# Kernel optimization log

Hardware: AMD Instinct MI355X
Metric: run time of the kernel (lower is better)

The kernel has to match this reference:

```python
import jax, jax.numpy as jnp
import numpy as np

B, C, H, W = 4, 128, 96, 96
OC = 128          # out_channels
K = 3             # kernel_size
OFF = 2 * K * K   # offset channels = 18
PAD = 1
EPS = 1e-6


def conv2d(x, w, b, pad=1, groups=1):
    out = jax.lax.conv_general_dilated(
        x, w, window_strides=(1, 1), padding=[(pad, pad), (pad, pad)],
        dimension_numbers=('NCHW', 'OIHW', 'NCHW'), feature_group_count=groups)
    return out + b[None, :, None, None]


def bilinear_gather(x, ys, xs):
    # x: [B,C,H,W]; ys, xs: [B,H,W] float sample coords. Zero outside bounds.
    Bn, Cn, Hn, Wn = x.shape
    xflat = x.reshape(Bn, Cn, Hn * Wn)
    y0 = jnp.floor(ys)
    x0 = jnp.floor(xs)
    out = jnp.zeros((Bn, Cn, Hn, Wn), dtype=x.dtype)
    for dy, dx in ((0, 0), (0, 1), (1, 0), (1, 1)):
        yy = y0 + dy
        xx = x0 + dx
        w = (1.0 - jnp.abs(ys - yy)) * (1.0 - jnp.abs(xs - xx))
        valid = (yy >= 0) & (yy < Hn) & (xx >= 0) & (xx < Wn)
        yi = jnp.clip(yy, 0, Hn - 1).astype(jnp.int32)
        xi = jnp.clip(xx, 0, Wn - 1).astype(jnp.int32)
        idx = (yi * Wn + xi).reshape(Bn, 1, Hn * Wn)
        g = jnp.take_along_axis(xflat, idx, axis=2).reshape(Bn, Cn, Hn, Wn)
        out = out + (w * valid)[:, None] * g
    return out


def deform_conv(x, offsets, w, b):
    # torchvision DeformConv2d v1: offsets [B, 2*K*K, H, W], pairs (dy, dx) per tap
    Bn, Cn, Hn, Wn = x.shape
    off = offsets.reshape(Bn, K * K, 2, Hn, Wn)
    gy, gx = jnp.meshgrid(jnp.arange(Hn, dtype=x.dtype),
                          jnp.arange(Wn, dtype=x.dtype), indexing='ij')
    acc = jnp.zeros((Bn, w.shape[0], Hn, Wn), dtype=x.dtype)
    for k in range(K * K):
        ky, kx = k // K, k % K
        ys = gy[None] - PAD + ky + off[:, k, 0]
        xs = gx[None] - PAD + kx + off[:, k, 1]
        samp = bilinear_gather(x, ys, xs)                 # [B,C,H,W]
        acc = acc + jnp.einsum('bchw,oc->bohw', samp, w[:, :, ky, kx])
    return acc + b[None, :, None, None]


def setup_inputs() -> dict:
    key = jax.random.key(0)
    ks = jax.random.split(key, 8)
    s = 0.05
    return {
        'x': jax.random.normal(ks[0], (B, C, H, W), jnp.float32),
        'w_off': jax.random.normal(ks[1], (OFF, C, K, K), jnp.float32) * s,
        'b_off': jnp.zeros((OFF,), jnp.float32),
        'w_def': jax.random.normal(ks[2], (OC, C, K, K), jnp.float32) * s,
        'b_def': jnp.zeros((OC,), jnp.float32),
        'ln_w': jnp.ones((OC,), jnp.float32),
        'ln_b': jnp.zeros((OC,), jnp.float32),
        'w_dw': jax.random.normal(ks[3], (C, 1, 3, 3), jnp.float32) * s,
        'b_dw': jnp.zeros((C,), jnp.float32),
        'w_pw': jax.random.normal(ks[4], (OC, C, 1, 1), jnp.float32) * s,
        'b_pw': jnp.zeros((OC,), jnp.float32),
    }


def reference(x, w_off, b_off, w_def, b_def, ln_w, ln_b, w_dw, b_dw, w_pw, b_pw):
    offsets = conv2d(x, w_off, b_off, pad=PAD)            # [B,18,H,W]
    x1 = deform_conv(x, offsets, w_def, b_def)            # [B,OC,H,W]
    # channels-first LayerNorm
    u = x1.mean(1, keepdims=True)
    s = ((x1 - u) ** 2).mean(1, keepdims=True)
    x1 = ln_w[None, :, None, None] * ((x1 - u) / jnp.sqrt(s + EPS)) \
         + ln_b[None, :, None, None]
    x2 = conv2d(x, w_dw, b_dw, pad=1, groups=C)           # depthwise 3x3
    x4 = conv2d(x2 + x, w_pw, b_pw, pad=0)                # pointwise 1x1
    x4 = jax.nn.silu(x4)
    return x1 + x4
```

## Files before the change

### kernel.cpp

```cpp
#include <hip/hip_runtime.h>
#include <hip/hip_bf16.h>
#include <stdint.h>

#define BN 4
#define CN 128
#define HN 96
#define WN 96
#define HW (HN*WN)
#define OCN 128
#define OFFC 18
#define EPSV 1e-6f
#define HP 98
#define WP 98

typedef __attribute__((ext_vector_type(8))) short bf16x8;
typedef __attribute__((ext_vector_type(4))) float f32x4;

__device__ __forceinline__ float lo16(uint32_t u) {
  union { uint32_t i; float f; } v; v.i = u << 16; return v.f;
}
__device__ __forceinline__ float hi16(uint32_t u) {
  union { uint32_t i; float f; } v; v.i = u & 0xffff0000u; return v.f;
}
__device__ __forceinline__ uint16_t f2b(float f) {
  union { float f; uint32_t i; } u; u.f = f;
  uint32_t r = u.i + 0x7fffu + ((u.i >> 16) & 1u);
  return (uint16_t)(r >> 16);
}
__device__ __forceinline__ uint32_t pk2(float a, float b) {
  return (uint32_t)f2b(a) | ((uint32_t)f2b(b) << 16);
}
__device__ __forceinline__ int swz(int row, int c) { return c ^ ((row & 7) << 3); }

__device__ __align__(16) uint16_t g_def[9 * 128 * 128];
__device__ __align__(16) uint16_t g_pw[128 * 128];
__device__ __align__(16) uint16_t g_off[32 * 1152];
__device__ __align__(16) uint16_t g_xp[(size_t)BN * HP * WP * CN];

__global__ __launch_bounds__(256)
void k_prep_w(const float* __restrict__ w_def, const float* __restrict__ w_pw,
              const float* __restrict__ w_off) {
  int i = blockIdx.x * 256 + threadIdx.x;
  if (i < 147456) {
    int k = i >> 14, rem = i & 16383, oc = rem >> 7, c = rem & 127;
    g_def[i] = f2b(w_def[((oc << 7) + c) * 9 + k]);
  } else if (i < 147456 + 16384) {
    int j = i - 147456;
    g_pw[j] = f2b(w_pw[j]);
  } else if (i < 147456 + 16384 + 36864) {
    int j = i - 163840;
    int row = j / 1152, col = j - row * 1152;
    int kk = col >> 7, c = col & 127;
    g_off[j] = (row < OFFC) ? f2b(w_off[((row << 7) + c) * 9 + kk]) : (uint16_t)0;
  }
}

__global__ __launch_bounds__(256)
void k_prep_x(const float* __restrict__ x) {
  __shared__ uint16_t trans[96][136];
  int blk = blockIdx.x;
  int y1 = blk % HP;
  int b  = blk / HP;
  int t = (int)threadIdx.x;
  uint16_t* dst = g_xp + ((size_t)(b * HP + y1) * WP) * CN;
  if (y1 == 0 || y1 == HP - 1) {
    for (int i = t; i < WP * CN / 8; i += 256)
      ((uint4*)dst)[i] = make_uint4(0, 0, 0, 0);
    return;
  }
  int y = y1 - 1;
  for (int i = t; i < CN * WN / 4; i += 256) {
    int c = i / 24, xq = i - c * 24;
    float4 f = *(const float4*)&x[((size_t)(b * CN + c) * HN + y) * WN + xq * 4];
    trans[xq * 4 + 0][c] = f2b(f.x);
    trans[xq * 4 + 1][c] = f2b(f.y);
    trans[xq * 4 + 2][c] = f2b(f.z);
    trans[xq * 4 + 3][c] = f2b(f.w);
  }
  __syncthreads();
  for (int i = t; i < 2 * CN / 8; i += 256) {
    int side = i >> 4, j = i & 15;
    ((uint4*)(dst + (size_t)side * (WP - 1) * CN))[j] = make_uint4(0, 0, 0, 0);
  }
  for (int i = t; i < WN * CN / 8; i += 256) {
    int xw = i >> 4, cq = (i & 15) * 8;
    ((uint4*)(dst + CN))[i] = *(const uint4*)&trans[xw][cq];
  }
}

__global__ __launch_bounds__(256, 3)
void k_fused(const float* __restrict__ b_off, const float* __restrict__ b_def,
             const float* __restrict__ ln_w, const float* __restrict__ ln_b,
             const float* __restrict__ w_dw, const float* __restrict__ b_dw,
             const float* __restrict__ b_pw, float* __restrict__ out) {
  __shared__ __align__(16) uint16_t patch[3 * 34 * 128];
  __shared__ float offarena[576];
  float (*offl)[32] = (float (*)[32])offarena;
  float (*red1)[32] = (float (*)[32])offarena;
  float (*red2)[32] = (float (*)[32])(offarena + 128);
  float* muv = offarena + 256;
  float* rsv = offarena + 288;
  uint16_t* samp0 = patch;
  uint16_t* samp1 = patch + 4096;
  uint16_t* dwT   = patch + 8192;

  int bid = blockIdx.x;
  int wid = (bid & 7) * 144 + (bid >> 3);
  int wt = wid % 3;
  int h  = (wid / 3) % HN;
  int b  = wid / (3 * HN);
  int w0 = wt * 32;

  int t = (int)threadIdx.x;
  int l = t & 63, w = t >> 6;
  int g = l >> 4, fr = l & 15;
  int p = t & 31, cg = t >> 5;
  const uint16_t* xb = g_xp + (size_t)b * HP * WP * CN;
  int cbase = w * 32 + (l & 3) * 8;
  const uint16_t* bp = xb + cbase;

  #pragma unroll
  for (int rep = 0; rep < 7; ++rep) {
    int e = t + 256 * rep;
    if (e < 1632) {
      int rec = e >> 4, chunk = e & 15;
      int ky = rec / 34, i = rec - 34 * ky;
      const uint16_t* src = xb + ((size_t)(h + ky) * WP + (w0 + i)) * CN + chunk * 8;
      *(uint4*)&patch[((ky * 34 + i) << 7) + swz(i, chunk * 8)] = *(const uint4*)src;
    }
  }
  __syncthreads();

  {
    int toc = w >> 1, tp = w & 1;
    f32x4 aco = {0.f, 0.f, 0.f, 0.f};
    #pragma unroll
    for (int ks = 0; ks < 36; ++ks) {
      int kk = ks >> 2;
      int ky = kk / 3, kx = kk - 3 * ky;
      int cb = ((ks & 3) << 5) + (g << 3);
      int i = fr + (tp << 4) + kx;
      bf16x8 a = *(const bf16x8*)&g_off[(toc * 16 + fr) * 1152 + (ks << 5) + (g << 3)];
      bf16x8 bb = *(const bf16x8*)&patch[((ky * 34 + i) << 7) + swz(i, cb)];
      aco = __builtin_amdgcn_mfma_f32_16x16x32_bf16(a, bb, aco, 0, 0, 0);
    }
    #pragma unroll
    for (int reg = 0; reg < 4; ++reg) {
      int j = toc * 16 + g * 4 + reg;
      if (j < OFFC) offl[j][(tp << 4) + fr] = aco[reg] + b_off[j];
    }
  }

  float adw[16];
  {
    #pragma unroll
    for (int cl = 0; cl < 16; ++cl) adw[cl] = b_dw[cg * 16 + cl];
    #pragma unroll
    for (int ky = 0; ky < 3; ++ky) {
      #pragma unroll
      for (int kx = 0; kx < 3; ++kx) {
        int i = p + kx;
        uint32_t r[8];
        *(uint4*)&r[0] = *(const uint4*)&patch[((ky * 34 + i) << 7) + swz(i, cg * 16)];
        *(uint4*)&r[4] = *(const uint4*)&patch[((ky * 34 + i) << 7) + swz(i, cg * 16 + 8)];
        #pragma unroll
        for (int c2 = 0; c2 < 8; ++c2) {
          adw[2 * c2]     += lo16(r[c2]) * w_dw[(cg * 16 + 2 * c2) * 9 + ky * 3 + kx];
          adw[2 * c2 + 1] += hi16(r[c2]) * w_dw[(cg * 16 + 2 * c2 + 1) * 9 + ky * 3 + kx];
        }
      }
    }
    int i = p + 1;
    uint32_t r[8];
    *(uint4*)&r[0] = *(const uint4*)&patch[((34 + i) << 7) + swz(i, cg * 16)];
    *(uint4*)&r[4] = *(const uint4*)&patch[((34 + i) << 7) + swz(i, cg * 16 + 8)];
    #pragma unroll
    for (int c2 = 0; c2 < 8; ++c2) {
      adw[2 * c2]     += lo16(r[c2]);
      adw[2 * c2 + 1] += hi16(r[c2]);
    }
  }
  __syncthreads();

  auto GATHER = [&](int kk, uint16_t* wb) {
    int ky = kk / 3, kx = kk - 3 * ky;
    #pragma unroll
    for (int half = 0; half < 2; ++half) {
      int px = half * 16 + (l >> 2);
      float dy = offl[2 * kk][px], dx = offl[2 * kk + 1][px];
      float ys = (float)(h - 1 + ky) + dy;
      float xs = (float)(w0 + px - 1 + kx) + dx;
      float y0f = floorf(ys), x0f = floorf(xs);
      float fy = ys - y0f, fx = xs - x0f;
      int y0 = (int)y0f, x0 = (int)x0f;
      float w00 = (1.f - fy) * (1.f - fx), w01 = (1.f - fy) * fx;
      float w10 = fy * (1.f - fx),         w11 = fy * fx;
      bool yok0 = (y0 >= 0) & (y0 < HN), yok1 = (y0 + 1 >= 0) & (y0 + 1 < HN);
      bool xok0 = (x0 >= 0) & (x0 < WN), xok1 = (x0 + 1 >= 0) & (x0 + 1 < WN);
      if (!(yok0 & xok0)) w00 = 0.f;
      if (!(yok0 & xok1)) w01 = 0.f;
      if (!(yok1 & xok0)) w10 = 0.f;
      if (!(yok1 & xok1)) w11 = 0.f;
      int ya  = min(max(y0, -1), HN) + 1;
      int yb2 = min(max(y0 + 1, -1), HN) + 1;
      int xa  = min(max(x0, -1), WN) + 1;
      int xc2 = min(max(x0 + 1, -1), WN) + 1;
      uint32_t A[4], B[4], C[4], D[4];
      *(uint4*)A = *(const uint4*)(bp + ((size_t)ya * WP + xa) * CN);
      *(uint4*)B = *(const uint4*)(bp + ((size_t)ya * WP + xc2) * CN);
      *(uint4*)C = *(const uint4*)(bp + ((size_t)yb2 * WP + xa) * CN);
      *(uint4*)D = *(const uint4*)(bp + ((size_t)yb2 * WP + xc2) * CN);
      uint32_t pk4[4];
      #pragma unroll
      for (int q2 = 0; q2 < 4; ++q2) {
        float s0 = w00 * lo16(A[q2]) + w01 * lo16(B[q2]) + w10 * lo16(C[q2]) + w11 * lo16(D[q2]);
        float s1 = w00 * hi16(A[q2]) + w01 * hi16(B[q2]) + w10 * hi16(C[q2]) + w11 * hi16(D[q2]);
        pk4[q2] = pk2(s0, s1);
      }
      *(uint4*)&wb[(px << 7) + swz(px, cbase)] = *(uint4*)pk4;
    }
  };

  {
    #pragma unroll
    for (int m = 0; m < 2; ++m) {
      uint4 u = { pk2(adw[8*m+0], adw[8*m+1]), pk2(adw[8*m+2], adw[8*m+3]),
                  pk2(adw[8*m+4], adw[8*m+5]), pk2(adw[8*m+6], adw[8*m+7]) };
      *(uint4*)&dwT[(p << 7) + swz(p, cg * 16 + 8 * m)] = u;
    }
    GATHER(0, samp0);
  }
  __syncthreads();

  f32x4 a4[2][2];
  #pragma unroll
  for (int q1 = 0; q1 < 2; ++q1)
    #pragma unroll
    for (int q2 = 0; q2 < 2; ++q2) a4[q1][q2] = (f32x4){0.f, 0.f, 0.f, 0.f};
  {
    #pragma unroll
    for (int ks = 0; ks < 4; ++ks) {
      int kb = (ks << 5) + (g << 3);
      bf16x8 a0 = *(const bf16x8*)&g_pw[(32 * w + fr) * 128 + kb];
      bf16x8 a1 = *(const bf16x8*)&g_pw[(32 * w + 16 + fr) * 128 + kb];
      #pragma unroll
      for (int tp2 = 0; tp2 < 2; ++tp2) {
        int pp = (tp2 << 4) + fr;
        bf16x8 bb = *(const bf16x8*)&dwT[(pp << 7) + swz(pp, kb)];
        a4[0][tp2] = __builtin_amdgcn_mfma_f32_16x16x32_bf16(a0, bb, a4[0][tp2], 0, 0, 0);
        a4[1][tp2] = __builtin_amdgcn_mfma_f32_16x16x32_bf16(a1, bb, a4[1][tp2], 0, 0, 0);
      }
    }
    #pragma unroll
    for (int toc2 = 0; toc2 < 2; ++toc2)
      #pragma unroll
      for (int tp2 = 0; tp2 < 2; ++tp2)
        #pragma unroll
        for (int reg = 0; reg < 4; ++reg) {
          int oc = 32 * w + 16 * toc2 + 4 * g + reg;
          float v = a4[toc2][tp2][reg] + b_pw[oc];
          a4[toc2][tp2][reg] = v / (1.f + __expf(-v));
        }
  }
  __syncthreads();

  f32x4 ac1[2][2];
  #pragma unroll
  for (int q1 = 0; q1 < 2; ++q1)
    #pragma unroll
    for (int q2 = 0; q2 < 2; ++q2) ac1[q1][q2] = (f32x4){0.f, 0.f, 0.f, 0.f};

  #pragma unroll 1
  for (int k = 0; k < 9; ++k) {
    uint16_t* rb = (k & 1) ? samp1 : samp0;
    uint16_t* wb = (k & 1) ? samp0 : samp1;
    if (k < 8) GATHER(k + 1, wb);
    {
      const uint16_t* gdk = g_def + (k << 14);
      #pragma unroll
      for (int ks = 0; ks < 4; ++ks) {
        int kb = (ks << 5) + (g << 3);
        bf16x8 a0 = *(const bf16x8*)&gdk[(32 * w + fr) * 128 + kb];
        bf16x8 a1 = *(const bf16x8*)&gdk[(32 * w + 16 + fr) * 128 + kb];
        #pragma unroll
        for (int tp2 = 0; tp2 < 2; ++tp2) {
          int pp = (tp2 << 4) + fr;
          bf16x8 bb = *(const bf16x8*)&rb[(pp << 7) + swz(pp, kb)];
          ac1[0][tp2] = __builtin_amdgcn_mfma_f32_16x16x32_bf16(a0, bb, ac1[0][tp2], 0, 0, 0);
          ac1[1][tp2] = __builtin_amdgcn_mfma_f32_16x16x32_bf16(a1, bb, ac1[1][tp2], 0, 0, 0);
        }
      }
    }
    __syncthreads();
  }

  #pragma unroll
  for (int toc2 = 0; toc2 < 2; ++toc2)
    #pragma unroll
    for (int tp2 = 0; tp2 < 2; ++tp2)
      #pragma unroll
      for (int reg = 0; reg < 4; ++reg) {
        int oc = 32 * w + 16 * toc2 + 4 * g + reg;
        ac1[toc2][tp2][reg] += b_def[oc];
      }
  {
    float s1[2], s2[2];
    #pragma unroll
    for (int tp2 = 0; tp2 < 2; ++tp2) {
      float a = 0.f, q = 0.f;
      #pragma unroll
      for (int toc2 = 0; toc2 < 2; ++toc2)
        #pragma unroll
        for (int reg = 0; reg < 4; ++reg) {
          float v = ac1[toc2][tp2][reg];
          a += v; q += v * v;
        }
      a += __shfl_xor(a, 16); a += __shfl_xor(a, 32);
      q += __shfl_xor(q, 16); q += __shfl_xor(q, 32);
      s1[tp2] = a; s2[tp2] = q;
    }
    if (l < 16) {
      red1[w][l] = s1[0]; red1[w][l + 16] = s1[1];
      red2[w][l] = s2[0]; red2[w][l + 16] = s2[1];
    }
  }
  __syncthreads();
  if (t < 32) {
    float m = (red1[0][t] + red1[1][t] + red1[2][t] + red1[3][t]) * (1.f / 128.f);
    float q = (red2[0][t] + red2[1][t] + red2[2][t] + red2[3][t]) * (1.f / 128.f) - m * m;
    muv[t] = m;
    rsv[t] = rsqrtf(q + EPSV);
  }
  __syncthreads();
  {
    #pragma unroll
    for (int toc2 = 0; toc2 < 2; ++toc2)
      #pragma unroll
      for (int tp2 = 0; tp2 < 2; ++tp2) {
        int pp = (tp2 << 4) + fr;
        float mm = muv[pp], rr = rsv[pp];
        #pragma unroll
        for (int reg = 0; reg < 4; ++reg) {
          int oc = 32 * w + 16 * toc2 + 4 * g + reg;
          float v = (ac1[toc2][tp2][reg] - mm) * rr * ln_w[oc] + ln_b[oc]
                    + a4[toc2][tp2][reg];
          out[((size_t)(b * OCN + oc) * HN + h) * WN + w0 + pp] = v;
        }
      }
  }
}

extern "C" void kernel_launch(void* const* d_in, const int* in_sizes, int n_in,
                              void* d_out, int out_size, void* d_ws, size_t ws_size,
                              hipStream_t stream) {
  const float* x     = (const float*)d_in[0];
  const float* w_off = (const float*)d_in[1];
  const float* b_off = (const float*)d_in[2];
  const float* w_def = (const float*)d_in[3];
  const float* b_def = (const float*)d_in[4];
  const float* ln_w  = (const float*)d_in[5];
  const float* ln_b  = (const float*)d_in[6];
  const float* w_dw  = (const float*)d_in[7];
  const float* b_dw  = (const float*)d_in[8];
  const float* w_pw  = (const float*)d_in[9];
  const float* b_pw  = (const float*)d_in[10];
  float* out = (float*)d_out;

  hipLaunchKernelGGL(k_prep_w, dim3(784), dim3(256), 0, stream, w_def, w_pw, w_off);
  hipLaunchKernelGGL(k_prep_x, dim3(BN * HP), dim3(256), 0, stream, x);
  hipLaunchKernelGGL(k_fused, dim3(BN * HN * 3), dim3(256), 0, stream,
                     b_off, b_def, ln_w, ln_b, w_dw, b_dw, b_pw, out);
}
```

Measured before the change: 116.7 us.

## Split deform conv reduction over channels per wave with private LDS buffers

Each wave now gathers and multiplies only its own 32-channel slice across all 128 output channels, using per-wave sample buffers. This removes the block-wide barrier after every tap. Partial sums are then reduced across the four waves through LDS in four serialized phases. In exchange each wave holds 64 accumulator floats, which raises register pressure, and the launch-bounds occupancy hint is dropped. The reduction also adds LDS traffic and extra barriers.

```diff
diff --git a/kernel.cpp b/kernel.cpp
--- a/kernel.cpp
+++ b/kernel.cpp
@@ -12,6 +12,7 @@
 #define EPSV 1e-6f
 #define HP 98
 #define WP 98
+#define NWG (BN*HN*3)
 
 typedef __attribute__((ext_vector_type(8))) short bf16x8;
 typedef __attribute__((ext_vector_type(4))) float f32x4;
@@ -88,21 +89,20 @@
   }
 }
 
-__global__ __launch_bounds__(256, 3)
+__global__ __launch_bounds__(256)
 void k_fused(const float* __restrict__ b_off, const float* __restrict__ b_def,
              const float* __restrict__ ln_w, const float* __restrict__ ln_b,
              const float* __restrict__ w_dw, const float* __restrict__ b_dw,
              const float* __restrict__ b_pw, float* __restrict__ out) {
-  __shared__ __align__(16) uint16_t patch[3 * 34 * 128];
+  __shared__ __align__(16) uint16_t patch[13056];
+  __shared__ __align__(16) uint16_t dwT[4096];
   __shared__ float offarena[576];
   float (*offl)[32] = (float (*)[32])offarena;
   float (*red1)[32] = (float (*)[32])offarena;
   float (*red2)[32] = (float (*)[32])(offarena + 128);
   float* muv = offarena + 256;
   float* rsv = offarena + 288;
-  uint16_t* samp0 = patch;
-  uint16_t* samp1 = patch + 4096;
-  uint16_t* dwT   = patch + 8192;
+  float* redbuf = (float*)patch;
 
   int bid = blockIdx.x;
   int wid = (bid & 7) * 144 + (bid >> 3);
@@ -118,6 +118,8 @@
   const uint16_t* xb = g_xp + (size_t)b * HP * WP * CN;
   int cbase = w * 32 + (l & 3) * 8;
   const uint16_t* bp = xb + cbase;
+  uint16_t* sbuf0 = patch + w * 1280;
+  uint16_t* sbuf1 = patch + 5120 + w * 1280;
 
   #pragma unroll
   for (int rep = 0; rep < 7; ++rep) {
@@ -184,6 +186,7 @@
 
   auto GATHER = [&](int kk, uint16_t* wb) {
     int ky = kk / 3, kx = kk - 3 * ky;
+    int chunk = l & 3;
     #pragma unroll
     for (int half = 0; half < 2; ++half) {
       int px = half * 16 + (l >> 2);
@@ -217,7 +220,24 @@
         float s1 = w00 * hi16(A[q2]) + w01 * hi16(B[q2]) + w10 * hi16(C[q2]) + w11 * hi16(D[q2]);
         pk4[q2] = pk2(s0, s1);
       }
-      *(uint4*)&wb[(px << 7) + swz(px, cbase)] = *(uint4*)pk4;
+      *(uint4*)&wb[px * 40 + chunk * 8] = *(uint4*)pk4;
+    }
+  };
+
+  f32x4 acc[8][2];
+  #pragma unroll
+  for (int r = 0; r < 8; ++r)
+    #pragma unroll
+    for (int q2 = 0; q2 < 2; ++q2) acc[r][q2] = (f32x4){0.f, 0.f, 0.f, 0.f};
+  auto TAPMM = [&](int k, const uint16_t* rb) {
+    const uint16_t* gdk = g_def + (k << 14) + w * 32 + g * 8;
+    bf16x8 b0 = *(const bf16x8*)&rb[fr * 40 + g * 8];
+    bf16x8 b1 = *(const bf16x8*)&rb[(16 + fr) * 40 + g * 8];
+    #pragma unroll
+    for (int r = 0; r < 8; ++r) {
+      bf16x8 a = *(const bf16x8*)&gdk[(16 * r + fr) * 128];
+      acc[r][0] = __builtin_amdgcn_mfma_f32_16x16x32_bf16(a, b0, acc[r][0], 0, 0, 0);
+      acc[r][1] = __builtin_amdgcn_mfma_f32_16x16x32_bf16(a, b1, acc[r][1], 0, 0, 0);
     }
   };
 
@@ -228,7 +248,7 @@
                   pk2(adw[8*m+4], adw[8*m+5]), pk2(adw[8*m+6], adw[8*m+7]) };
       *(uint4*)&dwT[(p << 7) + swz(p, cg * 16 + 8 * m)] = u;
     }
-    GATHER(0, samp0);
+    GATHER(0, sbuf0);
   }
   __syncthreads();
 
@@ -262,47 +282,47 @@
           a4[toc2][tp2][reg] = v / (1.f + __expf(-v));
         }
   }
-  __syncthreads();
+
+  #pragma unroll 1
+  for (int k = 0; k < 9; ++k) {
+    uint16_t* rb = (k & 1) ? sbuf1 : sbuf0;
+    uint16_t* wb = (k & 1) ? sbuf0 : sbuf1;
+    if (k < 8) GATHER(k + 1, wb);
+    TAPMM(k, rb);
+  }
+  __syncthreads();
+
+  #pragma unroll 1
+  for (int ph = 0; ph < 4; ++ph) {
+    if (w == ph) {
+      #pragma unroll
+      for (int r = 0; r < 8; ++r)
+        #pragma unroll
+        for (int tp2 = 0; tp2 < 2; ++tp2)
+          #pragma unroll
+          for (int reg = 0; reg < 4; ++reg) {
+            int oc = 16 * r + g * 4 + reg;
+            int px = 16 * tp2 + fr;
+            int idx = oc * 33 + px;
+            if (ph == 0) redbuf[idx] = acc[r][tp2][reg];
+            else         redbuf[idx] += acc[r][tp2][reg];
+          }
+    }
+    __syncthreads();
+  }
 
   f32x4 ac1[2][2];
   #pragma unroll
-  for (int q1 = 0; q1 < 2; ++q1)
-    #pragma unroll
-    for (int q2 = 0; q2 < 2; ++q2) ac1[q1][q2] = (f32x4){0.f, 0.f, 0.f, 0.f};
-
-  #pragma unroll 1
-  for (int k = 0; k < 9; ++k) {
-    uint16_t* rb = (k & 1) ? samp1 : samp0;
-    uint16_t* wb = (k & 1) ? samp0 : samp1;
-    if (k < 8) GATHER(k + 1, wb);
-    {
-      const uint16_t* gdk = g_def + (k << 14);
-      #pragma unroll
-      for (int ks = 0; ks < 4; ++ks) {
-        int kb = (ks << 5) + (g << 3);
-        bf16x8 a0 = *(const bf16x8*)&gdk[(32 * w + fr) * 128 + kb];
-        bf16x8 a1 = *(const bf16x8*)&gdk[(32 * w + 16 + fr) * 128 + kb];
-        #pragma unroll
-        for (int tp2 = 0; tp2 < 2; ++tp2) {
-          int pp = (tp2 << 4) + fr;
-          bf16x8 bb = *(const bf16x8*)&rb[(pp << 7) + swz(pp, kb)];
-          ac1[0][tp2] = __builtin_amdgcn_mfma_f32_16x16x32_bf16(a0, bb, ac1[0][tp2], 0, 0, 0);
-          ac1[1][tp2] = __builtin_amdgcn_mfma_f32_16x16x32_bf16(a1, bb, ac1[1][tp2], 0, 0, 0);
-        }
-      }
-    }
-    __syncthreads();
-  }
-
-  #pragma unroll
   for (int toc2 = 0; toc2 < 2; ++toc2)
     #pragma unroll
     for (int tp2 = 0; tp2 < 2; ++tp2)
       #pragma unroll
       for (int reg = 0; reg < 4; ++reg) {
         int oc = 32 * w + 16 * toc2 + 4 * g + reg;
-        ac1[toc2][tp2][reg] += b_def[oc];
-      }
+        int px = 16 * tp2 + fr;
+        ac1[toc2][tp2][reg] = redbuf[oc * 33 + px] + b_def[oc];
+      }
+
   {
     float s1[2], s2[2];
     #pragma unroll
@@ -319,6 +339,7 @@
       q += __shfl_xor(q, 16); q += __shfl_xor(q, 32);
       s1[tp2] = a; s2[tp2] = q;
     }
+    __syncthreads();
     if (l < 16) {
       red1[w][l] = s1[0]; red1[w][l + 16] = s1[1];
       red2[w][l] = s2[0]; red2[w][l + 16] = s2[1];
@@ -368,6 +389,6 @@
 
   hipLaunchKernelGGL(k_prep_w, dim3(784), dim3(256), 0, stream, w_def, w_pw, w_off);
   hipLaunchKernelGGL(k_prep_x, dim3(BN * HP), dim3(256), 0, stream, x);
-  hipLaunchKernelGGL(k_fused, dim3(BN * HN * 3), dim3(256), 0, stream,
+  hipLaunchKernelGGL(k_fused, dim3(NWG), dim3(256), 0, stream,
                      b_off, b_def, ln_w, ln_b, w_dw, b_dw, b_pw, out);
 }
```

Measured after the change: 216.5 us. 85.5% more time.

## Process two output rows per workgroup to reuse patch rows and weight fragments

Applied to the files above, without the earlier changes.

Each workgroup now computes two adjacent output rows instead of one. It loads a 4-row input patch shared by both rows and reuses the deform-conv weight fragments across the two rows inside an 18-step gather/MFMA pipeline. The aim is to cut redundant patch loads and weight reads from global memory and to halve the number of workgroups. In exchange it uses more registers and LDS, and the occupancy hint drops from 3 to 2 blocks per CU, with only 576 workgroups left to fill the GPU.

```diff
diff --git a/kernel.cpp b/kernel.cpp
--- a/kernel.cpp
+++ b/kernel.cpp
@@ -12,6 +12,7 @@
 #define EPSV 1e-6f
 #define HP 98
 #define WP 98
+#define NWG2 (BN*(HN/2)*3)
 
 typedef __attribute__((ext_vector_type(8))) short bf16x8;
 typedef __attribute__((ext_vector_type(4))) float f32x4;
@@ -88,27 +89,24 @@
   }
 }
 
-__global__ __launch_bounds__(256, 3)
+__global__ __launch_bounds__(256, 2)
 void k_fused(const float* __restrict__ b_off, const float* __restrict__ b_def,
              const float* __restrict__ ln_w, const float* __restrict__ ln_b,
              const float* __restrict__ w_dw, const float* __restrict__ b_dw,
              const float* __restrict__ b_pw, float* __restrict__ out) {
-  __shared__ __align__(16) uint16_t patch[3 * 34 * 128];
-  __shared__ float offarena[576];
-  float (*offl)[32] = (float (*)[32])offarena;
-  float (*red1)[32] = (float (*)[32])offarena;
-  float (*red2)[32] = (float (*)[32])(offarena + 128);
-  float* muv = offarena + 256;
-  float* rsv = offarena + 288;
-  uint16_t* samp0 = patch;
-  uint16_t* samp1 = patch + 4096;
-  uint16_t* dwT   = patch + 8192;
+  __shared__ __align__(16) uint16_t patch[4 * 34 * 128];
+  __shared__ float offarena[1152];
+
+  uint16_t* dwT   = patch;
+  uint16_t* samp0 = patch + 8192;
+  uint16_t* samp1 = patch + 12288;
 
   int bid = blockIdx.x;
-  int wid = (bid & 7) * 144 + (bid >> 3);
+  int wid = (bid & 7) * (NWG2 / 8) + (bid >> 3);
   int wt = wid % 3;
-  int h  = (wid / 3) % HN;
-  int b  = wid / (3 * HN);
+  int h2 = (wid / 3) % (HN / 2);
+  int b  = wid / (3 * (HN / 2));
+  int h  = 2 * h2;
   int w0 = wt * 32;
 
   int t = (int)threadIdx.x;
@@ -120,9 +118,9 @@
   const uint16_t* bp = xb + cbase;
 
   #pragma unroll
-  for (int rep = 0; rep < 7; ++rep) {
+  for (int rep = 0; rep < 9; ++rep) {
     int e = t + 256 * rep;
-    if (e < 1632) {
+    if (e < 2176) {
       int rec = e >> 4, chunk = e & 15;
       int ky = rec / 34, i = rec - 34 * ky;
       const uint16_t* src = xb + ((size_t)(h + ky) * WP + (w0 + i)) * CN + chunk * 8;
@@ -132,63 +130,71 @@
   __syncthreads();
 
   {
-    int toc = w >> 1, tp = w & 1;
-    f32x4 aco = {0.f, 0.f, 0.f, 0.f};
+    int t1 = w >> 1, toc = w & 1;
+    f32x4 aco0 = {0.f,0.f,0.f,0.f}, aco1 = {0.f,0.f,0.f,0.f};
     #pragma unroll
     for (int ks = 0; ks < 36; ++ks) {
       int kk = ks >> 2;
       int ky = kk / 3, kx = kk - 3 * ky;
       int cb = ((ks & 3) << 5) + (g << 3);
-      int i = fr + (tp << 4) + kx;
       bf16x8 a = *(const bf16x8*)&g_off[(toc * 16 + fr) * 1152 + (ks << 5) + (g << 3)];
-      bf16x8 bb = *(const bf16x8*)&patch[((ky * 34 + i) << 7) + swz(i, cb)];
-      aco = __builtin_amdgcn_mfma_f32_16x16x32_bf16(a, bb, aco, 0, 0, 0);
+      int i0 = fr + kx, i1 = fr + 16 + kx;
+      bf16x8 bb0 = *(const bf16x8*)&patch[(((t1 + ky) * 34 + i0) << 7) + swz(i0, cb)];
+      bf16x8 bb1 = *(const bf16x8*)&patch[(((t1 + ky) * 34 + i1) << 7) + swz(i1, cb)];
+      aco0 = __builtin_amdgcn_mfma_f32_16x16x32_bf16(a, bb0, aco0, 0, 0, 0);
+      aco1 = __builtin_amdgcn_mfma_f32_16x16x32_bf16(a, bb1, aco1, 0, 0, 0);
     }
     #pragma unroll
     for (int reg = 0; reg < 4; ++reg) {
       int j = toc * 16 + g * 4 + reg;
-      if (j < OFFC) offl[j][(tp << 4) + fr] = aco[reg] + b_off[j];
-    }
-  }
-
-  float adw[16];
-  {
-    #pragma unroll
-    for (int cl = 0; cl < 16; ++cl) adw[cl] = b_dw[cg * 16 + cl];
+      if (j < OFFC) {
+        offarena[t1 * 576 + j * 32 + fr]      = aco0[reg] + b_off[j];
+        offarena[t1 * 576 + j * 32 + 16 + fr] = aco1[reg] + b_off[j];
+      }
+    }
+  }
+
+  float adw0[16], adw1[16];
+  auto DW = [&](float (&A)[16], int t2) {
+    #pragma unroll
+    for (int cl = 0; cl < 16; ++cl) A[cl] = b_dw[cg * 16 + cl];
     #pragma unroll
     for (int ky = 0; ky < 3; ++ky) {
       #pragma unroll
       for (int kx = 0; kx < 3; ++kx) {
-        int i = p + kx;
+        int i = p + kx, row = t2 + ky;
         uint32_t r[8];
-        *(uint4*)&r[0] = *(const uint4*)&patch[((ky * 34 + i) << 7) + swz(i, cg * 16)];
-        *(uint4*)&r[4] = *(const uint4*)&patch[((ky * 34 + i) << 7) + swz(i, cg * 16 + 8)];
+        *(uint4*)&r[0] = *(const uint4*)&patch[((row * 34 + i) << 7) + swz(i, cg * 16)];
+        *(uint4*)&r[4] = *(const uint4*)&patch[((row * 34 + i) << 7) + swz(i, cg * 16 + 8)];
         #pragma unroll
         for (int c2 = 0; c2 < 8; ++c2) {
-          adw[2 * c2]     += lo16(r[c2]) * w_dw[(cg * 16 + 2 * c2) * 9 + ky * 3 + kx];
-          adw[2 * c2 + 1] += hi16(r[c2]) * w_dw[(cg * 16 + 2 * c2 + 1) * 9 + ky * 3 + kx];
+          A[2 * c2]     += lo16(r[c2]) * w_dw[(cg * 16 + 2 * c2) * 9 + ky * 3 + kx];
+          A[2 * c2 + 1] += hi16(r[c2]) * w_dw[(cg * 16 + 2 * c2 + 1) * 9 + ky * 3 + kx];
         }
       }
     }
-    int i = p + 1;
+    int i = p + 1, row = t2 + 1;
     uint32_t r[8];
-    *(uint4*)&r[0] = *(const uint4*)&patch[((34 + i) << 7) + swz(i, cg * 16)];
-    *(uint4*)&r[4] = *(const uint4*)&patch[((34 + i) << 7) + swz(i, cg * 16 + 8)];
+    *(uint4*)&r[0] = *(const uint4*)&patch[((row * 34 + i) << 7) + swz(i, cg * 16)];
+    *(uint4*)&r[4] = *(const uint4*)&patch[((row * 34 + i) << 7) + swz(i, cg * 16 + 8)];
     #pragma unroll
     for (int c2 = 0; c2 < 8; ++c2) {
-      adw[2 * c2]     += lo16(r[c2]);
-      adw[2 * c2 + 1] += hi16(r[c2]);
-    }
-  }
-  __syncthreads();
-
-  auto GATHER = [&](int kk, uint16_t* wb) {
+      A[2 * c2]     += lo16(r[c2]);
+      A[2 * c2 + 1] += hi16(r[c2]);
+    }
+  };
+  DW(adw0, 0);
+  DW(adw1, 1);
+  __syncthreads();
+
+  auto GATHER = [&](int kk, int t2, uint16_t* wb) {
     int ky = kk / 3, kx = kk - 3 * ky;
     #pragma unroll
     for (int half = 0; half < 2; ++half) {
       int px = half * 16 + (l >> 2);
-      float dy = offl[2 * kk][px], dx = offl[2 * kk + 1][px];
-      float ys = (float)(h - 1 + ky) + dy;
+      float dy = offarena[t2 * 576 + (2 * kk) * 32 + px];
+      float dx = offarena[t2 * 576 + (2 * kk + 1) * 32 + px];
+      float ys = (float)(h + t2 - 1 + ky) + dy;
       float xs = (float)(w0 + px - 1 + kx) + dx;
       float y0f = floorf(ys), x0f = floorf(xs);
       float fy = ys - y0f, fx = xs - x0f;
@@ -224,87 +230,117 @@
   {
     #pragma unroll
     for (int m = 0; m < 2; ++m) {
-      uint4 u = { pk2(adw[8*m+0], adw[8*m+1]), pk2(adw[8*m+2], adw[8*m+3]),
-                  pk2(adw[8*m+4], adw[8*m+5]), pk2(adw[8*m+6], adw[8*m+7]) };
-      *(uint4*)&dwT[(p << 7) + swz(p, cg * 16 + 8 * m)] = u;
-    }
-    GATHER(0, samp0);
-  }
-  __syncthreads();
-
-  f32x4 a4[2][2];
+      uint4 u0 = { pk2(adw0[8*m+0], adw0[8*m+1]), pk2(adw0[8*m+2], adw0[8*m+3]),
+                   pk2(adw0[8*m+4], adw0[8*m+5]), pk2(adw0[8*m+6], adw0[8*m+7]) };
+      *(uint4*)&dwT[(p << 7) + swz(p, cg * 16 + 8 * m)] = u0;
+      uint4 u1 = { pk2(adw1[8*m+0], adw1[8*m+1]), pk2(adw1[8*m+2], adw1[8*m+3]),
+                   pk2(adw1[8*m+4], adw1[8*m+5]), pk2(adw1[8*m+6], adw1[8*m+7]) };
+      *(uint4*)&dwT[4096 + (p << 7) + swz(p, cg * 16 + 8 * m)] = u1;
+    }
+    GATHER(0, 0, samp0);
+  }
+  __syncthreads();
+
+  f32x4 a4T0[2][2], a4T1[2][2];
   #pragma unroll
   for (int q1 = 0; q1 < 2; ++q1)
     #pragma unroll
-    for (int q2 = 0; q2 < 2; ++q2) a4[q1][q2] = (f32x4){0.f, 0.f, 0.f, 0.f};
+    for (int q2 = 0; q2 < 2; ++q2) {
+      a4T0[q1][q2] = (f32x4){0.f,0.f,0.f,0.f};
+      a4T1[q1][q2] = (f32x4){0.f,0.f,0.f,0.f};
+    }
   {
     #pragma unroll
     for (int ks = 0; ks < 4; ++ks) {
       int kb = (ks << 5) + (g << 3);
-      bf16x8 a0 = *(const bf16x8*)&g_pw[(32 * w + fr) * 128 + kb];
-      bf16x8 a1 = *(const bf16x8*)&g_pw[(32 * w + 16 + fr) * 128 + kb];
+      bf16x8 p0 = *(const bf16x8*)&g_pw[(32 * w + fr) * 128 + kb];
+      bf16x8 p1 = *(const bf16x8*)&g_pw[(32 * w + 16 + fr) * 128 + kb];
       #pragma unroll
       for (int tp2 = 0; tp2 < 2; ++tp2) {
         int pp = (tp2 << 4) + fr;
-        bf16x8 bb = *(const bf16x8*)&dwT[(pp << 7) + swz(pp, kb)];
-        a4[0][tp2] = __builtin_amdgcn_mfma_f32_16x16x32_bf16(a0, bb, a4[0][tp2], 0, 0, 0);
-        a4[1][tp2] = __builtin_amdgcn_mfma_f32_16x16x32_bf16(a1, bb, a4[1][tp2], 0, 0, 0);
-      }
-    }
+        bf16x8 bb0 = *(const bf16x8*)&dwT[(pp << 7) + swz(pp, kb)];
+        bf16x8 bb1 = *(const bf16x8*)&dwT[4096 + (pp << 7) + swz(pp, kb)];
+        a4T0[0][tp2] = __builtin_amdgcn_mfma_f32_16x16x32_bf16(p0, bb0, a4T0[0][tp2], 0, 0, 0);
+        a4T0[1][tp2] = __builtin_amdgcn_mfma_f32_16x16x32_bf16(p1, bb0, a4T0[1][tp2], 0, 0, 0);
+        a4T1[0][tp2] = __builtin_amdgcn_mfma_f32_16x16x32_bf16(p0, bb1, a4T1[0][tp2], 0, 0, 0);
+        a4T1[1][tp2] = __builtin_amdgcn_mfma_f32_16x16x32_bf16(p1, bb1, a4T1[1][tp2], 0, 0, 0);
+      }
+    }
+    auto SILU = [&](f32x4 (&A)[2][2]) {
+      #pragma unroll
+      for (int toc2 = 0; toc2 < 2; ++toc2)
+        #pragma unroll
+        for (int tp2 = 0; tp2 < 2; ++tp2)
+          #pragma unroll
+          for (int reg = 0; reg < 4; ++reg) {
+            int oc = 32 * w + 16 * toc2 + 4 * g + reg;
+            float v = A[toc2][tp2][reg] + b_pw[oc];
+            A[toc2][tp2][reg] = v / (1.f + __expf(-v));
+          }
+    };
+    SILU(a4T0); SILU(a4T1);
+  }
+  __syncthreads();
+
+  f32x4 acT0[2][2], acT1[2][2];
+  #pragma unroll
+  for (int q1 = 0; q1 < 2; ++q1)
+    #pragma unroll
+    for (int q2 = 0; q2 < 2; ++q2) {
+      acT0[q1][q2] = (f32x4){0.f,0.f,0.f,0.f};
+      acT1[q1][q2] = (f32x4){0.f,0.f,0.f,0.f};
+    }
+  bf16x8 af0[4], af1[4];
+  auto MM = [&](f32x4 (&A)[2][2], const uint16_t* rb) {
+    #pragma unroll
+    for (int ks = 0; ks < 4; ++ks) {
+      int kb = (ks << 5) + (g << 3);
+      #pragma unroll
+      for (int tp2 = 0; tp2 < 2; ++tp2) {
+        int pp = (tp2 << 4) + fr;
+        bf16x8 bb = *(const bf16x8*)&rb[(pp << 7) + swz(pp, kb)];
+        A[0][tp2] = __builtin_amdgcn_mfma_f32_16x16x32_bf16(af0[ks], bb, A[0][tp2], 0, 0, 0);
+        A[1][tp2] = __builtin_amdgcn_mfma_f32_16x16x32_bf16(af1[ks], bb, A[1][tp2], 0, 0, 0);
+      }
+    }
+  };
+
+  #pragma unroll 1
+  for (int s = 0; s < 18; ++s) {
+    int k = s >> 1;
+    uint16_t* rb = (s & 1) ? samp1 : samp0;
+    uint16_t* wb = (s & 1) ? samp0 : samp1;
+    if (s < 17) {
+      int sn = s + 1;
+      GATHER(sn >> 1, sn & 1, wb);
+    }
+    if ((s & 1) == 0) {
+      const uint16_t* gdk = g_def + (k << 14);
+      #pragma unroll
+      for (int ks = 0; ks < 4; ++ks) {
+        int kb = (ks << 5) + (g << 3);
+        af0[ks] = *(const bf16x8*)&gdk[(32 * w + fr) * 128 + kb];
+        af1[ks] = *(const bf16x8*)&gdk[(32 * w + 16 + fr) * 128 + kb];
+      }
+      MM(acT0, rb);
+    } else {
+      MM(acT1, rb);
+    }
+    __syncthreads();
+  }
+
+  auto ADDB = [&](f32x4 (&A)[2][2]) {
     #pragma unroll
     for (int toc2 = 0; toc2 < 2; ++toc2)
       #pragma unroll
       for (int tp2 = 0; tp2 < 2; ++tp2)
         #pragma unroll
-        for (int reg = 0; reg < 4; ++reg) {
-          int oc = 32 * w + 16 * toc2 + 4 * g + reg;
-          float v = a4[toc2][tp2][reg] + b_pw[oc];
-          a4[toc2][tp2][reg] = v / (1.f + __expf(-v));
-        }
-  }
-  __syncthreads();
-
-  f32x4 ac1[2][2];
-  #pragma unroll
-  for (int q1 = 0; q1 < 2; ++q1)
-    #pragma unroll
-    for (int q2 = 0; q2 < 2; ++q2) ac1[q1][q2] = (f32x4){0.f, 0.f, 0.f, 0.f};
-
-  #pragma unroll 1
-  for (int k = 0; k < 9; ++k) {
-    uint16_t* rb = (k & 1) ? samp1 : samp0;
-    uint16_t* wb = (k & 1) ? samp0 : samp1;
-    if (k < 8) GATHER(k + 1, wb);
-    {
-      const uint16_t* gdk = g_def + (k << 14);
-      #pragma unroll
-      for (int ks = 0; ks < 4; ++ks) {
-        int kb = (ks << 5) + (g << 3);
-        bf16x8 a0 = *(const bf16x8*)&gdk[(32 * w + fr) * 128 + kb];
-        bf16x8 a1 = *(const bf16x8*)&gdk[(32 * w + 16 + fr) * 128 + kb];
-        #pragma unroll
-        for (int tp2 = 0; tp2 < 2; ++tp2) {
-          int pp = (tp2 << 4) + fr;
-          bf16x8 bb = *(const bf16x8*)&rb[(pp << 7) + swz(pp, kb)];
-          ac1[0][tp2] = __builtin_amdgcn_mfma_f32_16x16x32_bf16(a0, bb, ac1[0][tp2], 0, 0, 0);
-          ac1[1][tp2] = __builtin_amdgcn_mfma_f32_16x16x32_bf16(a1, bb, ac1[1][tp2], 0, 0, 0);
-        }
-      }
-    }
-    __syncthreads();
-  }
-
-  #pragma unroll
-  for (int toc2 = 0; toc2 < 2; ++toc2)
-    #pragma unroll
-    for (int tp2 = 0; tp2 < 2; ++tp2)
-      #pragma unroll
-      for (int reg = 0; reg < 4; ++reg) {
-        int oc = 32 * w + 16 * toc2 + 4 * g + reg;
-        ac1[toc2][tp2][reg] += b_def[oc];
-      }
-  {
-    float s1[2], s2[2];
+        for (int reg = 0; reg < 4; ++reg)
+          A[toc2][tp2][reg] += b_def[32 * w + 16 * toc2 + 4 * g + reg];
+  };
+  ADDB(acT0); ADDB(acT1);
+
+  auto SUMS = [&](f32x4 (&A)[2][2], int t2) {
     #pragma unroll
     for (int tp2 = 0; tp2 < 2; ++tp2) {
       float a = 0.f, q = 0.f;
@@ -312,42 +348,51 @@
       for (int toc2 = 0; toc2 < 2; ++toc2)
         #pragma unroll
         for (int reg = 0; reg < 4; ++reg) {
-          float v = ac1[toc2][tp2][reg];
+          float v = A[toc2][tp2][reg];
           a += v; q += v * v;
         }
       a += __shfl_xor(a, 16); a += __shfl_xor(a, 32);
       q += __shfl_xor(q, 16); q += __shfl_xor(q, 32);
-      s1[tp2] = a; s2[tp2] = q;
-    }
-    if (l < 16) {
-      red1[w][l] = s1[0]; red1[w][l + 16] = s1[1];
-      red2[w][l] = s2[0]; red2[w][l + 16] = s2[1];
-    }
-  }
-  __syncthreads();
-  if (t < 32) {
-    float m = (red1[0][t] + red1[1][t] + red1[2][t] + red1[3][t]) * (1.f / 128.f);
-    float q = (red2[0][t] + red2[1][t] + red2[2][t] + red2[3][t]) * (1.f / 128.f) - m * m;
-    muv[t] = m;
-    rsv[t] = rsqrtf(q + EPSV);
-  }
-  __syncthreads();
-  {
+      if (l < 16) {
+        float* r1 = offarena + t2 * 256;
+        float* r2 = r1 + 128;
+        r1[w * 32 + l + 16 * tp2] = a;
+        r2[w * 32 + l + 16 * tp2] = q;
+      }
+    }
+  };
+  SUMS(acT0, 0); SUMS(acT1, 1);
+  __syncthreads();
+  if (t < 64) {
+    int tt = t >> 5, px = t & 31;
+    float* r1 = offarena + tt * 256;
+    float* r2 = r1 + 128;
+    float m = (r1[px] + r1[32 + px] + r1[64 + px] + r1[96 + px]) * (1.f / 128.f);
+    float q = (r2[px] + r2[32 + px] + r2[64 + px] + r2[96 + px]) * (1.f / 128.f) - m * m;
+    offarena[512 + tt * 32 + px] = m;
+    offarena[576 + tt * 32 + px] = rsqrtf(q + EPSV);
+  }
+  __syncthreads();
+
+  auto STORE = [&](f32x4 (&A)[2][2], f32x4 (&P)[2][2], int t2) {
     #pragma unroll
     for (int toc2 = 0; toc2 < 2; ++toc2)
       #pragma unroll
       for (int tp2 = 0; tp2 < 2; ++tp2) {
         int pp = (tp2 << 4) + fr;
-        float mm = muv[pp], rr = rsv[pp];
+        float mm = offarena[512 + t2 * 32 + pp];
+        float rr = offarena[576 + t2 * 32 + pp];
         #pragma unroll
         for (int reg = 0; reg < 4; ++reg) {
           int oc = 32 * w + 16 * toc2 + 4 * g + reg;
-          float v = (ac1[toc2][tp2][reg] - mm) * rr * ln_w[oc] + ln_b[oc]
-                    + a4[toc2][tp2][reg];
-          out[((size_t)(b * OCN + oc) * HN + h) * WN + w0 + pp] = v;
+          float v = (A[toc2][tp2][reg] - mm) * rr * ln_w[oc] + ln_b[oc]
+                    + P[toc2][tp2][reg];
+          out[((size_t)(b * OCN + oc) * HN + h + t2) * WN + w0 + pp] = v;
         }
       }
-  }
+  };
+  STORE(acT0, a4T0, 0);
+  STORE(acT1, a4T1, 1);
 }
 
 extern "C" void kernel_launch(void* const* d_in, const int* in_sizes, int n_in,
@@ -368,6 +413,6 @@
 
   hipLaunchKernelGGL(k_prep_w, dim3(784), dim3(256), 0, stream, w_def, w_pw, w_off);
   hipLaunchKernelGGL(k_prep_x, dim3(BN * HP), dim3(256), 0, stream, x);
-  hipLaunchKernelGGL(k_fused, dim3(BN * HN * 3), dim3(256), 0, stream,
+  hipLaunchKernelGGL(k_fused, dim3(NWG2), dim3(256), 0, stream,
                      b_off, b_def, ln_w, ln_b, w_dw, b_dw, b_pw, out);
 }
```

Measured after the change: 114.0 us. 2.4% less time.
